# Kernel tuning notes

Measured on AMD Instinct MI355X. Metric: run time of the kernel, lower is better.

The kernel has to match this reference:

```python
import jax, jax.numpy as jnp
import numpy as np

N = 50000        # nodes
E = 800000       # edges (avg degree 16)
F_IN, F_HID, F_OUT = 128, 256, 256
G = 64           # graphs in batch
NEG_SLOPE_ATT = 0.2   # GATConv attention leaky relu
NEG_SLOPE_ACT = 0.01  # nn.LeakyReLU default


def setup_inputs() -> dict:
    key = jax.random.key(0)
    ks = jax.random.split(key, 12)
    x = jax.random.normal(ks[0], (N, F_IN), dtype=jnp.float32)
    edge_index = jax.random.randint(ks[1], (2, E), 0, N, dtype=jnp.int64)
    batch = jnp.sort(jax.random.randint(ks[2], (N,), 0, G, dtype=jnp.int64))
    def glorot(k, shape):
        fan = sum(shape)
        s = jnp.sqrt(6.0 / fan).astype(jnp.float32)
        return jax.random.uniform(k, shape, jnp.float32, -s, s)
    W1 = glorot(ks[3], (F_IN, F_HID))
    a_s1 = glorot(ks[4], (F_HID,))
    a_d1 = glorot(ks[5], (F_HID,))
    b1 = jnp.zeros((F_HID,), jnp.float32)
    W2 = glorot(ks[6], (F_HID, F_OUT))
    a_s2 = glorot(ks[7], (F_OUT,))
    a_d2 = glorot(ks[8], (F_OUT,))
    b2 = jnp.zeros((F_OUT,), jnp.float32)
    return dict(x=x, edge_index=edge_index, batch=batch,
                W1=W1, a_s1=a_s1, a_d1=a_d1, b1=b1,
                W2=W2, a_s2=a_s2, a_d2=a_d2, b2=b2)


def gat_conv(x, src, dst, W, a_s, a_d, b):
    """Single-head PyG GATConv (self-loops already appended to src/dst)."""
    n = x.shape[0]
    h = x @ W                                   # [N, D]
    alpha_src = h @ a_s                         # [N]
    alpha_dst = h @ a_d                         # [N]
    e = jax.nn.leaky_relu(alpha_src[src] + alpha_dst[dst], NEG_SLOPE_ATT)  # [E+N]
    m = jax.ops.segment_max(e, dst, num_segments=n)
    p = jnp.exp(e - jax.lax.stop_gradient(m)[dst])
    denom = jax.ops.segment_sum(p, dst, num_segments=n)
    alpha = p / denom[dst]                      # softmax over incoming edges
    out = jax.ops.segment_sum(h[src] * alpha[:, None], dst, num_segments=n)
    return out + b


def reference(x, edge_index, batch, W1, a_s1, a_d1, b1, W2, a_s2, a_d2, b2):
    n = x.shape[0]
    loops = jnp.arange(n, dtype=edge_index.dtype)   # GATConv add_self_loops=True
    src = jnp.concatenate([edge_index[0], loops])
    dst = jnp.concatenate([edge_index[1], loops])
    h = gat_conv(x, src, dst, W1, a_s1, a_d1, b1)
    h = jax.nn.leaky_relu(h, NEG_SLOPE_ACT)         # dropout is identity in eval
    node_emb = gat_conv(h, src, dst, W2, a_s2, a_d2, b2)
    graph_emb = jax.ops.segment_sum(node_emb, batch, num_segments=G)
    return node_emb, graph_emb
```

## Files before the change

### kernel.cpp

```cpp
#include <hip/hip_runtime.h>
#include <math.h>

#define NN 50000
#define NE 800000
#define F_IN 128
#define F_HID 256
#define NG 64
#define NPART 8
#define CSR_CHUNKS 128
#define SLOTS 64

typedef __bf16 bf16x8 __attribute__((ext_vector_type(8)));
typedef float f32x4 __attribute__((ext_vector_type(4)));
typedef float f32x2 __attribute__((ext_vector_type(2)));
typedef unsigned short u16x8 __attribute__((ext_vector_type(8)));

static __device__ __forceinline__ unsigned short f2bf(float f) {
    union { float f; unsigned u; } v; v.f = f;
    unsigned r = v.u + 0x7fff + ((v.u >> 16) & 1);
    return (unsigned short)(r >> 16);
}
static __device__ __forceinline__ float bf2f(unsigned short u) {
    union { unsigned u; float f; } v; v.u = ((unsigned)u) << 16;
    return v.f;
}
static __device__ __forceinline__ f32x2 bf2x2(unsigned u) {
    union { unsigned u; float f; } lo, hi;
    lo.u = u << 16;
    hi.u = u & 0xffff0000u;
    f32x2 r; r[0] = lo.f; r[1] = hi.f;
    return r;
}

template <int K, bool AF32>
__global__ __launch_bounds__(256)
void gemm_mfma(const void* __restrict__ Ap, const ushort* __restrict__ Wt,
               ushort* __restrict__ C16, const float* __restrict__ a_s,
               const float* __restrict__ a_d, float* __restrict__ as_out,
               float* __restrict__ ad_out, int M) {
    const ushort* A16 = (const ushort*)Ap;
    const float* A32 = (const float*)Ap;
    __shared__ ushort As[64 * 40];
    __shared__ ushort Bs[256 * 40];
    __shared__ float dps[4][64];
    __shared__ float dpd[4][64];
    const int t = threadIdx.x;
    const int bm = blockIdx.x * 64;
    const int wv = t >> 6, lane = t & 63;
    const int wn = wv * 64;
    const int lrow = lane & 15, quad = lane >> 4;
    const int srow = t >> 2;
    const int skp = (t & 3) << 3;

    f32x4 acc[4][4];
    #pragma unroll
    for (int i = 0; i < 4; ++i)
        #pragma unroll
        for (int j = 0; j < 4; ++j)
            #pragma unroll
            for (int r = 0; r < 4; ++r) acc[i][j][r] = 0.f;

    const int r0 = bm + srow;

    auto load_a = [&](int k0, u16x8& a0) {
        a0 = (u16x8)(0);
        if (r0 < M) {
            if (AF32) {
                const float* p = A32 + (size_t)r0 * K + k0 + skp;
                float4 f0 = *(const float4*)p, f1 = *(const float4*)(p + 4);
                a0[0]=f2bf(f0.x); a0[1]=f2bf(f0.y); a0[2]=f2bf(f0.z); a0[3]=f2bf(f0.w);
                a0[4]=f2bf(f1.x); a0[5]=f2bf(f1.y); a0[6]=f2bf(f1.z); a0[7]=f2bf(f1.w);
            } else {
                a0 = *(const u16x8*)(A16 + (size_t)r0 * K + k0 + skp);
            }
        }
    };
    auto load_b = [&](int k0, u16x8& b0, u16x8& b1, u16x8& b2, u16x8& b3) {
        b0 = *(const u16x8*)(Wt + (size_t)srow * K + k0 + skp);
        b1 = *(const u16x8*)(Wt + (size_t)(srow + 64) * K + k0 + skp);
        b2 = *(const u16x8*)(Wt + (size_t)(srow + 128) * K + k0 + skp);
        b3 = *(const u16x8*)(Wt + (size_t)(srow + 192) * K + k0 + skp);
    };

    u16x8 a0, b0, b1, b2, b3;
    load_a(0, a0);
    load_b(0, b0, b1, b2, b3);

    for (int k0 = 0; k0 < K; k0 += 32) {
        __syncthreads();
        *(u16x8*)(As + srow * 40 + skp) = a0;
        *(u16x8*)(Bs + srow * 40 + skp) = b0;
        *(u16x8*)(Bs + (srow + 64) * 40 + skp) = b1;
        *(u16x8*)(Bs + (srow + 128) * 40 + skp) = b2;
        *(u16x8*)(Bs + (srow + 192) * 40 + skp) = b3;
        __syncthreads();
        bool more = (k0 + 32) < K;
        u16x8 na0, nb0, nb1, nb2, nb3;
        if (more) {
            load_a(k0 + 32, na0);
            load_b(k0 + 32, nb0, nb1, nb2, nb3);
        }
        bf16x8 af[4], bf_[4];
        #pragma unroll
        for (int i = 0; i < 4; ++i)
            af[i] = *(const bf16x8*)(As + (i * 16 + lrow) * 40 + quad * 8);
        #pragma unroll
        for (int j = 0; j < 4; ++j)
            bf_[j] = *(const bf16x8*)(Bs + (wn + j * 16 + lrow) * 40 + quad * 8);
        #pragma unroll
        for (int i = 0; i < 4; ++i)
            #pragma unroll
            for (int j = 0; j < 4; ++j)
                acc[i][j] = __builtin_amdgcn_mfma_f32_16x16x32_bf16(
                    af[i], bf_[j], acc[i][j], 0, 0, 0);
        if (more) { a0 = na0; b0 = nb0; b1 = nb1; b2 = nb2; b3 = nb3; }
    }
    float asf[4], adf[4];
    #pragma unroll
    for (int j = 0; j < 4; ++j) {
        asf[j] = a_s[wn + j * 16 + lrow];
        adf[j] = a_d[wn + j * 16 + lrow];
    }
    #pragma unroll
    for (int i = 0; i < 4; ++i) {
        #pragma unroll
        for (int r = 0; r < 4; ++r) {
            float ps = 0.f, pd = 0.f;
            #pragma unroll
            for (int j = 0; j < 4; ++j) {
                ps += acc[i][j][r] * asf[j];
                pd += acc[i][j][r] * adf[j];
            }
            #pragma unroll
            for (int off = 8; off; off >>= 1) {
                ps += __shfl_xor(ps, off);
                pd += __shfl_xor(pd, off);
            }
            if (lrow == 0) {
                dps[wv][i * 16 + quad * 4 + r] = ps;
                dpd[wv][i * 16 + quad * 4 + r] = pd;
            }
        }
    }
    __syncthreads();
    if (t < 64 && bm + t < M) {
        as_out[bm + t] = dps[0][t] + dps[1][t] + dps[2][t] + dps[3][t];
        ad_out[bm + t] = dpd[0][t] + dpd[1][t] + dpd[2][t] + dpd[3][t];
    }
    #pragma unroll
    for (int i = 0; i < 4; ++i) {
        int gm0 = bm + i * 16 + quad * 4;
        #pragma unroll
        for (int j = 0; j < 4; ++j) {
            int gn = wn + j * 16 + lrow;
            #pragma unroll
            for (int r = 0; r < 4; ++r)
                if (gm0 + r < M) C16[(size_t)(gm0 + r) * 256 + gn] = f2bf(acc[i][j][r]);
        }
    }
}

__global__ void cvt_wts(const float* __restrict__ W1, ushort* __restrict__ Wt1,
                        const float* __restrict__ W2, ushort* __restrict__ Wt2) {
    int idx = blockIdx.x * blockDim.x + threadIdx.x;
    if (idx < 256 * F_IN) {
        int n = idx / F_IN, k = idx - n * F_IN;
        Wt1[idx] = f2bf(W1[(size_t)k * 256 + n]);
    } else if (idx < 256 * F_IN + 256 * F_HID) {
        int i2 = idx - 256 * F_IN;
        int n = i2 / F_HID, k = i2 - n * F_HID;
        Wt2[i2] = f2bf(W2[(size_t)k * 256 + n]);
    }
}

__global__ __launch_bounds__(256)
void scatter_part(const int* __restrict__ src, const int* __restrict__ dst,
                  int* __restrict__ cursor, int* __restrict__ src_sorted,
                  int E, int n) {
    const int p = blockIdx.x & (NPART - 1);
    const int c = blockIdx.x >> 3;
    const int T = E + n;
    const int chunk = (T + CSR_CHUNKS - 1) / CSR_CHUNKS;
    const int i0 = c * chunk;
    const int i1 = min(i0 + chunk, T);
    for (int i = i0 + (int)threadIdx.x; i < i1; i += 256) {
        int d = (i < E) ? dst[i] : (i - E);
        int pd = (d * NPART) / NN;
        if (pd == p) {
            int s = (i < E) ? src[i] : d;
            int pos = atomicAdd(&cursor[d], 1);
            if (pos < SLOTS) src_sorted[(size_t)d * SLOTS + pos] = s;
        }
    }
}

template <bool ACT, bool BF16OUT, bool POOL>
__global__ __launch_bounds__(256)
void agg_kernel(const ushort* __restrict__ h, const float* __restrict__ as,
                const float* __restrict__ ad, const int* __restrict__ degs,
                const int* __restrict__ src_sorted, const float* __restrict__ bias,
                float* __restrict__ out, ushort* __restrict__ out16,
                const int* __restrict__ batch, float* __restrict__ gemb, int n) {
    const int hw = threadIdx.x >> 5;
    const int lane = threadIdx.x & 63;
    const int hl = lane & 31;
    const int base = lane & 32;
    const int node = blockIdx.x * 8 + hw;
    __shared__ float vbuf[8][256];
    __shared__ int gids[8];

    const bool valid = node < n;
    int deg = 0, start = 0;
    float adn = 0.f;
    if (valid) {
        deg = min(degs[node], SLOTS);
        start = node * SLOTS;
        adn = ad[node];
    }

    int s_lane = 0;
    float e_lane = -INFINITY;
    if (valid && hl < deg) {
        s_lane = src_sorted[start + hl];
        float e = as[s_lane] + adn;
        e_lane = e > 0.f ? e : 0.2f * e;
    }
    float m = e_lane;
    for (int j = 32 + hl; j < deg; j += 32) {
        int s = src_sorted[start + j];
        float e = as[s] + adn;
        e = e > 0.f ? e : 0.2f * e;
        m = fmaxf(m, e);
    }
    #pragma unroll
    for (int off = 16; off; off >>= 1) m = fmaxf(m, __shfl_xor(m, off));
    float p_lane = __expf(e_lane - m);
    float denom = p_lane;
    for (int j = 32 + hl; j < deg; j += 32) {
        int s = src_sorted[start + j];
        float e = as[s] + adn;
        e = e > 0.f ? e : 0.2f * e;
        denom += __expf(e - m);
    }
    #pragma unroll
    for (int off = 16; off; off >>= 1) denom += __shfl_xor(denom, off);
    float inv = valid ? (1.f / denom) : 0.f;
    p_lane *= inv;

    const ushort* hrow = h + hl * 8;
    f32x2 acc2[4];
    #pragma unroll
    for (int q = 0; q < 4; ++q) { acc2[q][0] = 0.f; acc2[q][1] = 0.f; }
    const int degc = min(deg, 32);
    for (int j0 = 0; j0 < degc; j0 += 4) {
        float wa = __shfl(p_lane, base | j0);       int sa = __shfl(s_lane, base | j0);
        float wb = __shfl(p_lane, base | (j0 + 1)); int sb = __shfl(s_lane, base | (j0 + 1));
        float wc = __shfl(p_lane, base | (j0 + 2)); int sc = __shfl(s_lane, base | (j0 + 2));
        float wd = __shfl(p_lane, base | (j0 + 3)); int sd = __shfl(s_lane, base | (j0 + 3));
        wb = (j0 + 1 < degc) ? wb : 0.f;
        wc = (j0 + 2 < degc) ? wc : 0.f;
        wd = (j0 + 3 < degc) ? wd : 0.f;
        uint4 ra = *(const uint4*)(hrow + (size_t)sa * 256);
        uint4 rb = *(const uint4*)(hrow + (size_t)sb * 256);
        uint4 rc = *(const uint4*)(hrow + (size_t)sc * 256);
        uint4 rd = *(const uint4*)(hrow + (size_t)sd * 256);
        f32x2 wa2; wa2[0] = wa; wa2[1] = wa;
        f32x2 wb2; wb2[0] = wb; wb2[1] = wb;
        f32x2 wc2; wc2[0] = wc; wc2[1] = wc;
        f32x2 wd2; wd2[0] = wd; wd2[1] = wd;
        acc2[0] += wa2 * bf2x2(ra.x); acc2[1] += wa2 * bf2x2(ra.y);
        acc2[2] += wa2 * bf2x2(ra.z); acc2[3] += wa2 * bf2x2(ra.w);
        acc2[0] += wb2 * bf2x2(rb.x); acc2[1] += wb2 * bf2x2(rb.y);
        acc2[2] += wb2 * bf2x2(rb.z); acc2[3] += wb2 * bf2x2(rb.w);
        acc2[0] += wc2 * bf2x2(rc.x); acc2[1] += wc2 * bf2x2(rc.y);
        acc2[2] += wc2 * bf2x2(rc.z); acc2[3] += wc2 * bf2x2(rc.w);
        acc2[0] += wd2 * bf2x2(rd.x); acc2[1] += wd2 * bf2x2(rd.y);
        acc2[2] += wd2 * bf2x2(rd.z); acc2[3] += wd2 * bf2x2(rd.w);
    }
    if (deg > 32) {
        for (int j = 32; j < deg; ++j) {
            int s = src_sorted[start + j];
            float e = as[s] + adn;
            e = e > 0.f ? e : 0.2f * e;
            float w = __expf(e - m) * inv;
            uint4 r = *(const uint4*)(hrow + (size_t)s * 256);
            f32x2 w2; w2[0] = w; w2[1] = w;
            acc2[0] += w2 * bf2x2(r.x); acc2[1] += w2 * bf2x2(r.y);
            acc2[2] += w2 * bf2x2(r.z); acc2[3] += w2 * bf2x2(r.w);
        }
    }
    const float4* b4 = (const float4*)bias;
    float4 b0 = b4[hl * 2], b1 = b4[hl * 2 + 1];
    float v[8];
    v[0] = acc2[0][0] + b0.x; v[1] = acc2[0][1] + b0.y;
    v[2] = acc2[1][0] + b0.z; v[3] = acc2[1][1] + b0.w;
    v[4] = acc2[2][0] + b1.x; v[5] = acc2[2][1] + b1.y;
    v[6] = acc2[3][0] + b1.z; v[7] = acc2[3][1] + b1.w;
    if (ACT) {
        #pragma unroll
        for (int k = 0; k < 8; ++k) v[k] = v[k] > 0.f ? v[k] : 0.01f * v[k];
    }
    if (valid) {
        if (BF16OUT) {
            u16x8 o;
            #pragma unroll
            for (int k = 0; k < 8; ++k) o[k] = f2bf(v[k]);
            *(u16x8*)(out16 + (size_t)node * 256 + hl * 8) = o;
        } else {
            float4 o0 = make_float4(v[0], v[1], v[2], v[3]);
            float4 o1 = make_float4(v[4], v[5], v[6], v[7]);
            float4* op = (float4*)(out + (size_t)node * 256);
            op[hl * 2] = o0;
            op[hl * 2 + 1] = o1;
        }
    }
    if (POOL) {
        *(float4*)&vbuf[hw][hl * 8]     = make_float4(v[0], v[1], v[2], v[3]);
        *(float4*)&vbuf[hw][hl * 8 + 4] = make_float4(v[4], v[5], v[6], v[7]);
        if (hl == 0) gids[hw] = valid ? batch[node] : -1;
        __syncthreads();
        const int t = threadIdx.x;
        float acc = 0.f;
        int cur = gids[0];
        #pragma unroll
        for (int i = 0; i < 8; ++i) {
            int g = gids[i];
            if (g < 0) break;
            if (g != cur) {
                atomicAdd(&gemb[(size_t)cur * 256 + t], acc);
                acc = 0.f; cur = g;
            }
            acc += vbuf[i][t];
        }
        if (cur >= 0) atomicAdd(&gemb[(size_t)cur * 256 + t], acc);
    }
}

static inline char* align_up(char* p, size_t a) {
    return (char*)(((uintptr_t)p + a - 1) & ~(uintptr_t)(a - 1));
}

extern "C" void kernel_launch(void* const* d_in, const int* in_sizes, int n_in,
                              void* d_out, int out_size, void* d_ws, size_t ws_size,
                              hipStream_t stream) {
    const float* x     = (const float*)d_in[0];
    const int* eidx    = (const int*)d_in[1];
    const int* batch   = (const int*)d_in[2];
    const float* W1    = (const float*)d_in[3];
    const float* a_s1  = (const float*)d_in[4];
    const float* a_d1  = (const float*)d_in[5];
    const float* b1    = (const float*)d_in[6];
    const float* W2    = (const float*)d_in[7];
    const float* a_s2  = (const float*)d_in[8];
    const float* a_d2  = (const float*)d_in[9];
    const float* b2    = (const float*)d_in[10];

    float* node_emb  = (float*)d_out;
    float* graph_emb = node_emb + (size_t)NN * 256;

    char* ws = (char*)d_ws;
    ushort* h16  = (ushort*)ws;  ws += (size_t)NN * 256 * sizeof(ushort);
    ws = align_up(ws, 256);
    ushort* z16  = (ushort*)ws;  ws += (size_t)NN * 256 * sizeof(ushort);
    ws = align_up(ws, 256);
    ushort* wt1  = (ushort*)ws;  ws += (size_t)256 * F_IN * sizeof(ushort);
    ws = align_up(ws, 256);
    ushort* wt2  = (ushort*)ws;  ws += (size_t)256 * F_HID * sizeof(ushort);
    ws = align_up(ws, 256);
    float* as_buf = (float*)ws;  ws += (size_t)NN * sizeof(float);
    float* ad_buf = (float*)ws;  ws += (size_t)NN * sizeof(float);
    int* cursor   = (int*)ws;    ws += (size_t)NN * sizeof(int);
    ws = align_up(ws, 256);
    int* src_sorted = (int*)ws;  ws += (size_t)NN * SLOTS * sizeof(int);

    const int* e_src = eidx;
    const int* e_dst = eidx + NE;

    int gemm_blocks = (NN + 63) / 64;
    int agg_blocks = (NN + 7) / 8;

    hipMemsetAsync(cursor, 0, (size_t)NN * sizeof(int), stream);
    scatter_part<<<NPART * CSR_CHUNKS, 256, 0, stream>>>(e_src, e_dst, cursor, src_sorted, NE, NN);

    cvt_wts<<<(256 * (F_IN + F_HID) + 255) / 256, 256, 0, stream>>>(W1, wt1, W2, wt2);

    gemm_mfma<F_IN, true><<<gemm_blocks, 256, 0, stream>>>(x, wt1, h16, a_s1, a_d1, as_buf, ad_buf, NN);
    agg_kernel<true, true, false><<<agg_blocks, 256, 0, stream>>>(
        h16, as_buf, ad_buf, cursor, src_sorted, b1, nullptr, z16, nullptr, nullptr, NN);

    hipMemsetAsync(graph_emb, 0, (size_t)NG * 256 * sizeof(float), stream);
    gemm_mfma<F_HID, false><<<gemm_blocks, 256, 0, stream>>>(z16, wt2, h16, a_s2, a_d2, as_buf, ad_buf, NN);
    agg_kernel<false, false, true><<<agg_blocks, 256, 0, stream>>>(
        h16, as_buf, ad_buf, cursor, src_sorted, b2, node_emb, nullptr, batch, graph_emb, NN);
}
```

Baseline: 310.4 us.

## Load GEMM MFMA operands directly from global memory, dropping LDS staging

The GEMM kernel no longer stages A and W tiles through shared memory with two barriers per k-step. Each wave now loads its MFMA fragments straight from global memory (through cache), with A rows clamped instead of zero-filled. This removes LDS traffic and __syncthreads. In exchange, all four waves reload the same A fragments and the software double-buffer prefetch is gone, so more global/L2 traffic goes through the cache.

```diff
diff --git a/kernel.cpp b/kernel.cpp
--- a/kernel.cpp
+++ b/kernel.cpp
@@ -40,8 +40,6 @@
                float* __restrict__ ad_out, int M) {
     const ushort* A16 = (const ushort*)Ap;
     const float* A32 = (const float*)Ap;
-    __shared__ ushort As[64 * 40];
-    __shared__ ushort Bs[256 * 40];
     __shared__ float dps[4][64];
     __shared__ float dpd[4][64];
     const int t = threadIdx.x;
@@ -49,8 +47,7 @@
     const int wv = t >> 6, lane = t & 63;
     const int wn = wv * 64;
     const int lrow = lane & 15, quad = lane >> 4;
-    const int srow = t >> 2;
-    const int skp = (t & 3) << 3;
+    const int kq = quad * 8;
 
     f32x4 acc[4][4];
     #pragma unroll
@@ -60,60 +57,38 @@
             #pragma unroll
             for (int r = 0; r < 4; ++r) acc[i][j][r] = 0.f;
 
-    const int r0 = bm + srow;
-
-    auto load_a = [&](int k0, u16x8& a0) {
-        a0 = (u16x8)(0);
-        if (r0 < M) {
+    int arow[4], brow[4];
+    #pragma unroll
+    for (int i = 0; i < 4; ++i) {
+        arow[i] = min(bm + i * 16 + lrow, M - 1);
+        brow[i] = wn + i * 16 + lrow;
+    }
+
+    #pragma unroll 2
+    for (int k0 = 0; k0 < K; k0 += 32) {
+        bf16x8 af[4], bf_[4];
+        #pragma unroll
+        for (int i = 0; i < 4; ++i) {
             if (AF32) {
-                const float* p = A32 + (size_t)r0 * K + k0 + skp;
+                const float* p = A32 + (size_t)arow[i] * K + k0 + kq;
                 float4 f0 = *(const float4*)p, f1 = *(const float4*)(p + 4);
-                a0[0]=f2bf(f0.x); a0[1]=f2bf(f0.y); a0[2]=f2bf(f0.z); a0[3]=f2bf(f0.w);
-                a0[4]=f2bf(f1.x); a0[5]=f2bf(f1.y); a0[6]=f2bf(f1.z); a0[7]=f2bf(f1.w);
+                u16x8 a;
+                a[0]=f2bf(f0.x); a[1]=f2bf(f0.y); a[2]=f2bf(f0.z); a[3]=f2bf(f0.w);
+                a[4]=f2bf(f1.x); a[5]=f2bf(f1.y); a[6]=f2bf(f1.z); a[7]=f2bf(f1.w);
+                af[i] = *(const bf16x8*)&a;
             } else {
-                a0 = *(const u16x8*)(A16 + (size_t)r0 * K + k0 + skp);
-            }
-        }
-    };
-    auto load_b = [&](int k0, u16x8& b0, u16x8& b1, u16x8& b2, u16x8& b3) {
-        b0 = *(const u16x8*)(Wt + (size_t)srow * K + k0 + skp);
-        b1 = *(const u16x8*)(Wt + (size_t)(srow + 64) * K + k0 + skp);
-        b2 = *(const u16x8*)(Wt + (size_t)(srow + 128) * K + k0 + skp);
-        b3 = *(const u16x8*)(Wt + (size_t)(srow + 192) * K + k0 + skp);
-    };
-
-    u16x8 a0, b0, b1, b2, b3;
-    load_a(0, a0);
-    load_b(0, b0, b1, b2, b3);
-
-    for (int k0 = 0; k0 < K; k0 += 32) {
-        __syncthreads();
-        *(u16x8*)(As + srow * 40 + skp) = a0;
-        *(u16x8*)(Bs + srow * 40 + skp) = b0;
-        *(u16x8*)(Bs + (srow + 64) * 40 + skp) = b1;
-        *(u16x8*)(Bs + (srow + 128) * 40 + skp) = b2;
-        *(u16x8*)(Bs + (srow + 192) * 40 + skp) = b3;
-        __syncthreads();
-        bool more = (k0 + 32) < K;
-        u16x8 na0, nb0, nb1, nb2, nb3;
-        if (more) {
-            load_a(k0 + 32, na0);
-            load_b(k0 + 32, nb0, nb1, nb2, nb3);
-        }
-        bf16x8 af[4], bf_[4];
-        #pragma unroll
-        for (int i = 0; i < 4; ++i)
-            af[i] = *(const bf16x8*)(As + (i * 16 + lrow) * 40 + quad * 8);
+                af[i] = *(const bf16x8*)(A16 + (size_t)arow[i] * K + k0 + kq);
+            }
+        }
         #pragma unroll
         for (int j = 0; j < 4; ++j)
-            bf_[j] = *(const bf16x8*)(Bs + (wn + j * 16 + lrow) * 40 + quad * 8);
+            bf_[j] = *(const bf16x8*)(Wt + (size_t)brow[j] * K + k0 + kq);
         #pragma unroll
         for (int i = 0; i < 4; ++i)
             #pragma unroll
             for (int j = 0; j < 4; ++j)
                 acc[i][j] = __builtin_amdgcn_mfma_f32_16x16x32_bf16(
                     af[i], bf_[j], acc[i][j], 0, 0, 0);
-        if (more) { a0 = na0; b0 = nb0; b1 = nb1; b2 = nb2; b3 = nb3; }
     }
     float asf[4], adf[4];
     #pragma unroll
```

Result: slower. 339.5 us (+9.4%).
